# Kernel tuning notes

Hardware: AMD Instinct MI355X
Metric: run time of the kernel (lower is better)

The kernel has to match this reference:

```python
import jax, jax.numpy as jnp
import numpy as np

B, L, D, H = 4, 1024, 1024, 16
DH = D // H
NEG = -1e9


def setup_inputs() -> dict:
    key = jax.random.key(0)
    ks = jax.random.split(key, 8)
    sequence = jax.random.normal(ks[0], (B, L, D), dtype=jnp.float32)
    # additive padding mask: all tokens valid -> zeros
    padding_mask = jnp.zeros((B, 1, 1, L), dtype=jnp.float32)
    # additive causal dependency mask: -1e9 above the diagonal
    causal = jnp.triu(jnp.full((L, L), NEG, dtype=jnp.float32), k=1)
    dependency_mask = causal[None, None, :, :]
    scale = 1.0 / np.sqrt(D)
    Wq = jax.random.normal(ks[1], (D, D), dtype=jnp.float32) * scale
    Wk = jax.random.normal(ks[2], (D, D), dtype=jnp.float32) * scale
    Wv = jax.random.normal(ks[3], (D, D), dtype=jnp.float32) * scale
    bq = jnp.zeros((D,), dtype=jnp.float32)
    bk = jnp.zeros((D,), dtype=jnp.float32)
    bv = jnp.zeros((D,), dtype=jnp.float32)
    return {"sequence": sequence, "padding_mask": padding_mask,
            "dependency_mask": dependency_mask,
            "Wq": Wq, "bq": bq, "Wk": Wk, "bk": bk, "Wv": Wv, "bv": bv}


def reference(sequence, padding_mask, dependency_mask, Wq, bq, Wk, bk, Wv, bv):
    b, l, d = sequence.shape
    h, dh = H, d // H
    # Q/K/V linear projections (torch Linear: x @ W^T + b)
    q = (sequence @ Wq.T + bq).reshape(b, l, h, dh)
    k = (sequence @ Wk.T + bk).reshape(b, l, h, dh)
    v = (sequence @ Wv.T + bv).reshape(b, l, h, dh)
    # scaled dot-product scores: [B, H, L, L]
    scores = jnp.einsum('blhd,bmhd->bhlm', q, k) / jnp.sqrt(jnp.float32(dh))
    scores = scores + padding_mask + dependency_mask
    attn = jax.nn.softmax(scores, axis=-1)
    # dropout is identity in eval mode (training=False)
    out = jnp.einsum('bhlm,bmhd->blhd', attn, v)
    return out.reshape(b, l, d)
```

## Files before the change

### kernel.cpp

```cpp
#include <hip/hip_runtime.h>
#include <hip/hip_bf16.h>


#define LL 1024

typedef __attribute__((ext_vector_type(8))) short short8;
typedef __attribute__((ext_vector_type(4))) float floatx4;

__device__ __forceinline__ float bf2f(unsigned short u) {
    return __uint_as_float(((unsigned int)u) << 16);
}
__device__ __forceinline__ unsigned short f2bf(float f) {
    unsigned int x = __float_as_uint(f);
    unsigned int r = x + 0x7fffu + ((x >> 16) & 1u);
    return (unsigned short)(r >> 16);
}

#if __has_builtin(__builtin_amdgcn_global_load_lds)
#define HAVE_GLL 1
typedef __attribute__((address_space(1))) unsigned int as1_u32;
typedef __attribute__((address_space(3))) unsigned int as3_u32;
__device__ __forceinline__ void gll16(const void* g, void* l) {
    __builtin_amdgcn_global_load_lds((const as1_u32*)g, (as3_u32*)l, 16, 0, 0);
}
#endif

__global__ __launch_bounds__(256) void conv_in(
    const float* __restrict__ seq, const float* __restrict__ wq,
    const float* __restrict__ wk,  const float* __restrict__ wv,
    const float* __restrict__ bq,  const float* __restrict__ bk,
    const float* __restrict__ bv,  const float* __restrict__ pm,
    unsigned short* __restrict__ ws)
{
    unsigned int t = blockIdx.x * 256u + threadIdx.x;
    const float* src; unsigned int idx; unsigned short* dst; float scale = 1.0f;
    if (t < 4194304u)      { src = seq; idx = t;            dst = ws + 12582912u; }
    else if (t < 5242880u) { src = wq;  idx = t - 4194304u; dst = ws + 16777216u; }
    else if (t < 6291456u) { src = wk;  idx = t - 5242880u; dst = ws + 17825792u; }
    else if (t < 7340032u) { src = wv;  idx = t - 6291456u; dst = ws + 18874368u; }
    else if (t < 7341056u) { src = bq;  idx = t - 7340032u; dst = ws + 20971520u; }
    else if (t < 7342080u) { src = bk;  idx = t - 7341056u; dst = ws + 20972544u; }
    else if (t < 7343104u) { src = bv;  idx = t - 7342080u; dst = ws + 20973568u; }
    else { src = pm; idx = t - 7343104u; dst = ws + 20974592u; scale = 1.4426950f; }
    dst[idx] = f2bf(src[idx] * scale);
}

__global__ __launch_bounds__(256) void qkv_proj(
    const unsigned short* __restrict__ X,
    const unsigned short* __restrict__ Wq, const unsigned short* __restrict__ bq,
    const unsigned short* __restrict__ Wk, const unsigned short* __restrict__ bk,
    const unsigned short* __restrict__ Wv, const unsigned short* __restrict__ bv,
    unsigned short* __restrict__ dst_base)
{
    const int z = blockIdx.z;
    const unsigned short* W    = (z == 0) ? Wq : ((z == 1) ? Wk : Wv);
    const unsigned short* bias = (z == 0) ? bq : ((z == 1) ? bk : bv);
    const float osc = (z == 0) ? 0.18033688f : 1.0f;
    unsigned short* dst = dst_base + (size_t)z * (4096u * 1024u);

    __shared__ __align__(16) unsigned short AsF[8192];
    __shared__ __align__(16) unsigned short BsF[8192];

    const int tid  = threadIdx.x;
    const int lane = tid & 63;
    const int wave = tid >> 6;
    const int quad = lane >> 4, r16 = lane & 15;
    const int wr = wave >> 1, wc = wave & 1;
    const int m0 = blockIdx.x * 128;
    const int n0 = blockIdx.y * 128;

    const int st_r3  = lane >> 3;
    const int st_col = ((lane & 7) ^ st_r3) << 3;

    floatx4 acc[4][4];
#pragma unroll
    for (int i = 0; i < 4; ++i)
#pragma unroll
        for (int j = 0; j < 4; ++j)
#pragma unroll
            for (int r = 0; r < 4; ++r) acc[i][j][r] = 0.f;

    for (int k0 = 0; k0 < 1024; k0 += 64) {
        __syncthreads();
#ifdef HAVE_GLL
#pragma unroll
        for (int c2 = 0; c2 < 4; ++c2) {
            int seg = wave * 4 + c2;
            int row = seg * 8 + st_r3;
            gll16(X + (size_t)(m0 + row) * 1024 + k0 + st_col, &AsF[seg * 512]);
            gll16(W + (size_t)(n0 + row) * 1024 + k0 + st_col, &BsF[seg * 512]);
        }
#else
#pragma unroll
        for (int c2 = 0; c2 < 4; ++c2) {
            int seg = wave * 4 + c2;
            int row = seg * 8 + st_r3;
            *(uint4*)&AsF[seg * 512 + lane * 8] = *(const uint4*)(X + (size_t)(m0 + row) * 1024 + k0 + st_col);
            *(uint4*)&BsF[seg * 512 + lane * 8] = *(const uint4*)(W + (size_t)(n0 + row) * 1024 + k0 + st_col);
        }
#endif
        __syncthreads();

#pragma unroll
        for (int kk = 0; kk < 2; ++kk) {
            const int csw = ((kk * 4 + quad) ^ (r16 & 7)) << 3;
            short8 a[4], b[4];
#pragma unroll
            for (int i = 0; i < 4; ++i)
                a[i] = *(const short8*)&AsF[(wr * 64 + i * 16 + r16) * 64 + csw];
#pragma unroll
            for (int j = 0; j < 4; ++j)
                b[j] = *(const short8*)&BsF[(wc * 64 + j * 16 + r16) * 64 + csw];
#pragma unroll
            for (int i = 0; i < 4; ++i)
#pragma unroll
                for (int j = 0; j < 4; ++j)
                    acc[i][j] = __builtin_amdgcn_mfma_f32_16x16x32_bf16(a[i], b[j], acc[i][j], 0, 0, 0);
        }
    }

#pragma unroll
    for (int j = 0; j < 4; ++j) {
        int n = n0 + wc * 64 + j * 16 + r16;
        float bvf = bf2f(bias[n]);
        int h = n >> 6, d = n & 63;
#pragma unroll
        for (int i = 0; i < 4; ++i) {
            int m_base = m0 + wr * 64 + i * 16 + quad * 4;
            int b = m_base >> 10, l0 = m_base & 1023;
            if (z == 2) {
                ushort4 st;
                st.x = f2bf(acc[i][j][0] + bvf); st.y = f2bf(acc[i][j][1] + bvf);
                st.z = f2bf(acc[i][j][2] + bvf); st.w = f2bf(acc[i][j][3] + bvf);
                *(ushort4*)&dst[(((size_t)(b * 16 + h)) * 64 + d) * 1024 + l0] = st;
            } else {
#pragma unroll
                for (int r = 0; r < 4; ++r)
                    dst[(((size_t)(b * 16 + h)) * 1024 + (l0 + r)) * 64 + d] =
                        f2bf((acc[i][j][r] + bvf) * osc);
            }
        }
    }
}

__global__ __launch_bounds__(256) void attn(
    const unsigned short* __restrict__ Qw,
    const unsigned short* __restrict__ Kw,
    const unsigned short* __restrict__ Vt_g,
    const unsigned short* __restrict__ pmask,
    float* __restrict__ out)
{
    __shared__ __align__(16) unsigned short KsF[8192];
    __shared__ __align__(16) unsigned short VsF[8192];
    __shared__ __align__(16) unsigned short PsF[4][2048];

    const int tid  = threadIdx.x;
    const int lane = tid & 63;
    const int wave = tid >> 6;
    const int quad = lane >> 4, r16 = lane & 15;

    const int bid  = blockIdx.x;
    const int half = bid >> 8, rr = bid & 255;
    const int bh   = half * 32 + (rr >> 3);
    const int qi   = half ? (7 - (rr & 7)) : (rr & 7);
    const int b    = bh >> 4, h = bh & 15;
    const int q0   = qi << 7;

    const size_t base = (size_t)bh * (1024 * 64);
    const unsigned short* Qg = Qw + base;
    const unsigned short* Kg = Kw + base;
    const unsigned short* Vg = Vt_g + base;

    const int kst_r3  = lane >> 3;
    const int kst_col = ((lane & 7) ^ kst_r3) << 3;
    const int vst_r   = lane >> 4;

    short8 aq[2][2];
#pragma unroll
    for (int f = 0; f < 2; ++f) {
        int qrow = q0 + f * 64 + wave * 16 + r16;
        aq[f][0] = *(const short8*)(Qg + (size_t)qrow * 64 + quad * 8);
        aq[f][1] = *(const short8*)(Qg + (size_t)qrow * 64 + 32 + quad * 8);
    }

    float lsum[2][4];
    floatx4 o[2][4];
#pragma unroll
    for (int f = 0; f < 2; ++f)
#pragma unroll
        for (int r = 0; r < 4; ++r) lsum[f][r] = 0.f;
#pragma unroll
    for (int f = 0; f < 2; ++f)
#pragma unroll
        for (int j = 0; j < 4; ++j)
#pragma unroll
            for (int r = 0; r < 4; ++r) o[f][j][r] = 0.f;

    for (int kt = 0; kt <= qi; ++kt) {
        __syncthreads();
#ifdef HAVE_GLL
#pragma unroll
        for (int c2 = 0; c2 < 4; ++c2) {
            int seg = wave * 4 + c2;
            int krow = seg * 8 + kst_r3;
            gll16(Kg + (size_t)(kt * 128 + krow) * 64 + kst_col, &KsF[seg * 512]);
            int vrow = seg * 4 + vst_r;
            int vcol = (((lane & 15) ^ (vrow & 7))) << 3;
            gll16(Vg + (size_t)vrow * 1024 + kt * 128 + vcol, &VsF[seg * 512]);
        }
#else
#pragma unroll
        for (int c2 = 0; c2 < 4; ++c2) {
            int seg = wave * 4 + c2;
            int krow = seg * 8 + kst_r3;
            *(uint4*)&KsF[seg * 512 + lane * 8] =
                *(const uint4*)(Kg + (size_t)(kt * 128 + krow) * 64 + kst_col);
            int vrow = seg * 4 + vst_r;
            int vcol = (((lane & 15) ^ (vrow & 7))) << 3;
            *(uint4*)&VsF[seg * 512 + lane * 8] =
                *(const uint4*)(Vg + (size_t)vrow * 1024 + kt * 128 + vcol);
        }
#endif
        __syncthreads();

        float pm2[8];
#pragma unroll
        for (int j = 0; j < 8; ++j)
            pm2[j] = bf2f(pmask[b * LL + kt * 128 + j * 16 + r16]) - 12.0f;

#pragma unroll
        for (int f = 0; f < 2; ++f) {
            floatx4 s[8];
#pragma unroll
            for (int j = 0; j < 8; ++j)
#pragma unroll
                for (int r = 0; r < 4; ++r) s[j][r] = 0.f;
#pragma unroll
            for (int j = 0; j < 8; ++j) {
                short8 bk0 = *(const short8*)&KsF[(j * 16 + r16) * 64 + ((((0 * 4 + quad)) ^ (r16 & 7)) << 3)];
                s[j] = __builtin_amdgcn_mfma_f32_16x16x32_bf16(aq[f][0], bk0, s[j], 0, 0, 0);
                short8 bk1 = *(const short8*)&KsF[(j * 16 + r16) * 64 + ((((1 * 4 + quad)) ^ (r16 & 7)) << 3)];
                s[j] = __builtin_amdgcn_mfma_f32_16x16x32_bf16(aq[f][1], bk1, s[j], 0, 0, 0);
            }

            if (kt == qi) {
                const int my_q = q0 + f * 64 + wave * 16 + quad * 4;
#pragma unroll
                for (int j = 0; j < 8; ++j) {
                    int key = kt * 128 + j * 16 + r16;
#pragma unroll
                    for (int r = 0; r < 4; ++r)
                        if (key > my_q + r) s[j][r] -= 1.0e9f;
                }
            }

            asm volatile("s_waitcnt lgkmcnt(0)" ::: "memory");
#pragma unroll
            for (int j = 0; j < 8; ++j) {
                int key = j * 16 + r16;
                int ab = ((key >> 5) << 9) + (((key >> 3) & 3) << 7) + (key & 7) + (quad << 5);
#pragma unroll
                for (int r = 0; r < 4; ++r) {
                    float p = exp2f(s[j][r] + pm2[j]);
                    lsum[f][r] += p;
                    PsF[wave][ab + (r << 3)] = f2bf(p);
                }
            }
            asm volatile("s_waitcnt lgkmcnt(0)" ::: "memory");

#pragma unroll
            for (int kk4 = 0; kk4 < 4; ++kk4) {
                short8 ap = *(const short8*)&PsF[wave][kk4 * 512 + lane * 8];
#pragma unroll
                for (int j2 = 0; j2 < 4; ++j2) {
                    short8 bv = *(const short8*)&VsF[(j2 * 16 + r16) * 128 + (((kk4 * 4 + quad) ^ (r16 & 7)) << 3)];
                    o[f][j2] = __builtin_amdgcn_mfma_f32_16x16x32_bf16(ap, bv, o[f][j2], 0, 0, 0);
                }
            }
        }
    }

#pragma unroll
    for (int f = 0; f < 2; ++f) {
        float linv[4];
#pragma unroll
        for (int r = 0; r < 4; ++r) {
            float l = lsum[f][r];
            l += __shfl_xor(l, 1);
            l += __shfl_xor(l, 2);
            l += __shfl_xor(l, 4);
            l += __shfl_xor(l, 8);
            linv[r] = 1.0f / fmaxf(l, 1.0e-30f);
        }
        const int my_q = q0 + f * 64 + wave * 16 + quad * 4;
#pragma unroll
        for (int j2 = 0; j2 < 4; ++j2) {
            int d = j2 * 16 + r16;
#pragma unroll
            for (int r = 0; r < 4; ++r) {
                size_t oidx = ((size_t)(b * 1024 + my_q + r)) * 1024 + h * 64 + d;
                out[oidx] = o[f][j2][r] * linv[r];
            }
        }
    }
}

__global__ __launch_bounds__(256) void fill_sentinel_f(float* __restrict__ out,
                                                       float v, unsigned int n)
{
    unsigned int t = blockIdx.x * 256u + threadIdx.x;
    if (t < n) out[t] = v;
}

extern "C" void kernel_launch(void* const* d_in, const int* in_sizes, int n_in,
                              void* d_out, int out_size, void* d_ws, size_t ws_size,
                              hipStream_t stream) {
    bool sizes_ok = (n_in == 9) && in_sizes[0] == 4194304 && in_sizes[1] == 4096 &&
                    in_sizes[2] == 1048576 && in_sizes[3] == 1048576 && in_sizes[4] == 1024 &&
                    in_sizes[5] == 1048576 && in_sizes[6] == 1024 && in_sizes[7] == 1048576 &&
                    in_sizes[8] == 1024 && out_size == 4194304;
    if (!sizes_ok) {
        fill_sentinel_f<<<16384, 256, 0, stream>>>((float*)d_out, 100.0f, 4194304u);
        return;
    }
    if (ws_size < 50331652u) {
        fill_sentinel_f<<<16384, 256, 0, stream>>>((float*)d_out, 200.0f, 4194304u);
        return;
    }

    unsigned short* ws = (unsigned short*)d_ws;

    conv_in<<<28700, 256, 0, stream>>>(
        (const float*)d_in[0], (const float*)d_in[3], (const float*)d_in[5],
        (const float*)d_in[7], (const float*)d_in[4], (const float*)d_in[6],
        (const float*)d_in[8], (const float*)d_in[1], ws);

    const unsigned short* cseq = ws + 12582912u;
    const unsigned short* cwq  = ws + 16777216u;
    const unsigned short* cwk  = ws + 17825792u;
    const unsigned short* cwv  = ws + 18874368u;
    const unsigned short* cbq  = ws + 20971520u;
    const unsigned short* cbk  = ws + 20972544u;
    const unsigned short* cbv  = ws + 20973568u;
    const unsigned short* cpm  = ws + 20974592u;

    dim3 g1(32, 8, 3);
    qkv_proj<<<g1, 256, 0, stream>>>(cseq, cwq, cbq, cwk, cbk, cwv, cbv, ws);

    attn<<<512, 256, 0, stream>>>(ws, ws + 4194304u, ws + 8388608u, cpm, (float*)d_out);
}
```

Baseline: 174.8 us.

## Vectorize input conversion and restructure attention to 64-row tiles without LDS K/V

The fp32-to-bf16 conversion kernel now handles 8 elements per thread with float4 loads and a packed 16-byte store, cutting the launch to about an eighth of the blocks. The attention kernel switches from 128-query blocks with LDS-staged K/V tiles to 64-query blocks on a 2D grid. Each wave loads its K and V MFMA operands directly from global memory into registers, which removes the block-wide barriers. The P tile layout is changed to a padded row-major buffer. The cost is that every wave re-reads K/V from global/L2 instead of sharing them, register pressure rises, and blocks no longer pair causal tiles for load balance.

Result: slower. 264.1 us (+51.1%).

```diff
diff --git a/kernel.cpp b/kernel.cpp
--- a/kernel.cpp
+++ b/kernel.cpp
@@ -33,16 +33,25 @@
     unsigned short* __restrict__ ws)
 {
     unsigned int t = blockIdx.x * 256u + threadIdx.x;
+    if (t >= 918400u) return;
+    unsigned int e = t * 8u;
     const float* src; unsigned int idx; unsigned short* dst; float scale = 1.0f;
-    if (t < 4194304u)      { src = seq; idx = t;            dst = ws + 12582912u; }
-    else if (t < 5242880u) { src = wq;  idx = t - 4194304u; dst = ws + 16777216u; }
-    else if (t < 6291456u) { src = wk;  idx = t - 5242880u; dst = ws + 17825792u; }
-    else if (t < 7340032u) { src = wv;  idx = t - 6291456u; dst = ws + 18874368u; }
-    else if (t < 7341056u) { src = bq;  idx = t - 7340032u; dst = ws + 20971520u; }
-    else if (t < 7342080u) { src = bk;  idx = t - 7341056u; dst = ws + 20972544u; }
-    else if (t < 7343104u) { src = bv;  idx = t - 7342080u; dst = ws + 20973568u; }
-    else { src = pm; idx = t - 7343104u; dst = ws + 20974592u; scale = 1.4426950f; }
-    dst[idx] = f2bf(src[idx] * scale);
+    if (e < 4194304u)      { src = seq; idx = e;            dst = ws + 12582912u; }
+    else if (e < 5242880u) { src = wq;  idx = e - 4194304u; dst = ws + 16777216u; }
+    else if (e < 6291456u) { src = wk;  idx = e - 5242880u; dst = ws + 17825792u; }
+    else if (e < 7340032u) { src = wv;  idx = e - 6291456u; dst = ws + 18874368u; }
+    else if (e < 7341056u) { src = bq;  idx = e - 7340032u; dst = ws + 20971520u; }
+    else if (e < 7342080u) { src = bk;  idx = e - 7341056u; dst = ws + 20972544u; }
+    else if (e < 7343104u) { src = bv;  idx = e - 7342080u; dst = ws + 20973568u; }
+    else { src = pm; idx = e - 7343104u; dst = ws + 20974592u; scale = 1.4426950f; }
+    float4 a = *(const float4*)(src + idx);
+    float4 c = *(const float4*)(src + idx + 4);
+    uint4 st;
+    st.x = (unsigned)f2bf(a.x * scale) | ((unsigned)f2bf(a.y * scale) << 16);
+    st.y = (unsigned)f2bf(a.z * scale) | ((unsigned)f2bf(a.w * scale) << 16);
+    st.z = (unsigned)f2bf(c.x * scale) | ((unsigned)f2bf(c.y * scale) << 16);
+    st.w = (unsigned)f2bf(c.z * scale) | ((unsigned)f2bf(c.w * scale) << 16);
+    *(uint4*)(dst + idx) = st;
 }
 
 __global__ __launch_bounds__(256) void qkv_proj(
@@ -150,157 +159,118 @@
     const unsigned short* __restrict__ pmask,
     float* __restrict__ out)
 {
-    __shared__ __align__(16) unsigned short KsF[8192];
-    __shared__ __align__(16) unsigned short VsF[8192];
-    __shared__ __align__(16) unsigned short PsF[4][2048];
+    __shared__ __align__(16) unsigned short PsF[4][2176];
 
     const int tid  = threadIdx.x;
     const int lane = tid & 63;
     const int wave = tid >> 6;
     const int quad = lane >> 4, r16 = lane & 15;
 
-    const int bid  = blockIdx.x;
-    const int half = bid >> 8, rr = bid & 255;
-    const int bh   = half * 32 + (rr >> 3);
-    const int qi   = half ? (7 - (rr & 7)) : (rr & 7);
-    const int b    = bh >> 4, h = bh & 15;
-    const int q0   = qi << 7;
+    const int qt = blockIdx.x;
+    const int bh = blockIdx.y;
+    const int b  = bh >> 4, h = bh & 15;
+    const int q0 = qt * 64;
 
     const size_t base = (size_t)bh * (1024 * 64);
     const unsigned short* Qg = Qw + base;
     const unsigned short* Kg = Kw + base;
     const unsigned short* Vg = Vt_g + base;
 
-    const int kst_r3  = lane >> 3;
-    const int kst_col = ((lane & 7) ^ kst_r3) << 3;
-    const int vst_r   = lane >> 4;
-
-    short8 aq[2][2];
-#pragma unroll
-    for (int f = 0; f < 2; ++f) {
-        int qrow = q0 + f * 64 + wave * 16 + r16;
-        aq[f][0] = *(const short8*)(Qg + (size_t)qrow * 64 + quad * 8);
-        aq[f][1] = *(const short8*)(Qg + (size_t)qrow * 64 + 32 + quad * 8);
-    }
-
-    float lsum[2][4];
-    floatx4 o[2][4];
-#pragma unroll
-    for (int f = 0; f < 2; ++f)
-#pragma unroll
-        for (int r = 0; r < 4; ++r) lsum[f][r] = 0.f;
-#pragma unroll
-    for (int f = 0; f < 2; ++f)
-#pragma unroll
-        for (int j = 0; j < 4; ++j)
-#pragma unroll
-            for (int r = 0; r < 4; ++r) o[f][j][r] = 0.f;
-
-    for (int kt = 0; kt <= qi; ++kt) {
-        __syncthreads();
-#ifdef HAVE_GLL
-#pragma unroll
-        for (int c2 = 0; c2 < 4; ++c2) {
-            int seg = wave * 4 + c2;
-            int krow = seg * 8 + kst_r3;
-            gll16(Kg + (size_t)(kt * 128 + krow) * 64 + kst_col, &KsF[seg * 512]);
-            int vrow = seg * 4 + vst_r;
-            int vcol = (((lane & 15) ^ (vrow & 7))) << 3;
-            gll16(Vg + (size_t)vrow * 1024 + kt * 128 + vcol, &VsF[seg * 512]);
-        }
-#else
-#pragma unroll
-        for (int c2 = 0; c2 < 4; ++c2) {
-            int seg = wave * 4 + c2;
-            int krow = seg * 8 + kst_r3;
-            *(uint4*)&KsF[seg * 512 + lane * 8] =
-                *(const uint4*)(Kg + (size_t)(kt * 128 + krow) * 64 + kst_col);
-            int vrow = seg * 4 + vst_r;
-            int vcol = (((lane & 15) ^ (vrow & 7))) << 3;
-            *(uint4*)&VsF[seg * 512 + lane * 8] =
-                *(const uint4*)(Vg + (size_t)vrow * 1024 + kt * 128 + vcol);
-        }
-#endif
-        __syncthreads();
+    const int qrow = q0 + wave * 16 + r16;
+    short8 aq0 = *(const short8*)(Qg + (size_t)qrow * 64 + quad * 8);
+    short8 aq1 = *(const short8*)(Qg + (size_t)qrow * 64 + 32 + quad * 8);
+
+    const int my_q = q0 + wave * 16 + quad * 4;
+
+    float lsum[4];
+    floatx4 o[4];
+#pragma unroll
+    for (int r = 0; r < 4; ++r) lsum[r] = 0.f;
+#pragma unroll
+    for (int j2 = 0; j2 < 4; ++j2)
+#pragma unroll
+        for (int r = 0; r < 4; ++r) o[j2][r] = 0.f;
+
+    const int ktmax = qt >> 1;
+    for (int kt = 0; kt <= ktmax; ++kt) {
+        short8 bk[8][2];
+#pragma unroll
+        for (int j = 0; j < 8; ++j)
+#pragma unroll
+            for (int kk = 0; kk < 2; ++kk)
+                bk[j][kk] = *(const short8*)(Kg + (size_t)(kt * 128 + j * 16 + r16) * 64 + kk * 32 + quad * 8);
+
+        floatx4 s[8];
+#pragma unroll
+        for (int j = 0; j < 8; ++j)
+#pragma unroll
+            for (int r = 0; r < 4; ++r) s[j][r] = 0.f;
+#pragma unroll
+        for (int j = 0; j < 8; ++j) {
+            s[j] = __builtin_amdgcn_mfma_f32_16x16x32_bf16(aq0, bk[j][0], s[j], 0, 0, 0);
+            s[j] = __builtin_amdgcn_mfma_f32_16x16x32_bf16(aq1, bk[j][1], s[j], 0, 0, 0);
+        }
+
+        short8 bv[4][4];
+#pragma unroll
+        for (int j2 = 0; j2 < 4; ++j2)
+#pragma unroll
+            for (int kk4 = 0; kk4 < 4; ++kk4)
+                bv[j2][kk4] = *(const short8*)(Vg + (size_t)(j2 * 16 + r16) * 1024 + kt * 128 + kk4 * 32 + quad * 8);
 
         float pm2[8];
 #pragma unroll
         for (int j = 0; j < 8; ++j)
             pm2[j] = bf2f(pmask[b * LL + kt * 128 + j * 16 + r16]) - 12.0f;
 
-#pragma unroll
-        for (int f = 0; f < 2; ++f) {
-            floatx4 s[8];
-#pragma unroll
-            for (int j = 0; j < 8; ++j)
-#pragma unroll
-                for (int r = 0; r < 4; ++r) s[j][r] = 0.f;
+        if (kt == ktmax) {
 #pragma unroll
             for (int j = 0; j < 8; ++j) {
-                short8 bk0 = *(const short8*)&KsF[(j * 16 + r16) * 64 + ((((0 * 4 + quad)) ^ (r16 & 7)) << 3)];
-                s[j] = __builtin_amdgcn_mfma_f32_16x16x32_bf16(aq[f][0], bk0, s[j], 0, 0, 0);
-                short8 bk1 = *(const short8*)&KsF[(j * 16 + r16) * 64 + ((((1 * 4 + quad)) ^ (r16 & 7)) << 3)];
-                s[j] = __builtin_amdgcn_mfma_f32_16x16x32_bf16(aq[f][1], bk1, s[j], 0, 0, 0);
+                int key = kt * 128 + j * 16 + r16;
+#pragma unroll
+                for (int r = 0; r < 4; ++r)
+                    if (key > my_q + r) s[j][r] -= 1.0e9f;
             }
-
-            if (kt == qi) {
-                const int my_q = q0 + f * 64 + wave * 16 + quad * 4;
-#pragma unroll
-                for (int j = 0; j < 8; ++j) {
-                    int key = kt * 128 + j * 16 + r16;
-#pragma unroll
-                    for (int r = 0; r < 4; ++r)
-                        if (key > my_q + r) s[j][r] -= 1.0e9f;
-                }
+        }
+
+        asm volatile("s_waitcnt lgkmcnt(0)" ::: "memory");
+#pragma unroll
+        for (int j = 0; j < 8; ++j) {
+#pragma unroll
+            for (int r = 0; r < 4; ++r) {
+                float p = exp2f(s[j][r] + pm2[j]);
+                lsum[r] += p;
+                PsF[wave][(quad * 4 + r) * 136 + j * 16 + r16] = f2bf(p);
             }
-
-            asm volatile("s_waitcnt lgkmcnt(0)" ::: "memory");
-#pragma unroll
-            for (int j = 0; j < 8; ++j) {
-                int key = j * 16 + r16;
-                int ab = ((key >> 5) << 9) + (((key >> 3) & 3) << 7) + (key & 7) + (quad << 5);
-#pragma unroll
-                for (int r = 0; r < 4; ++r) {
-                    float p = exp2f(s[j][r] + pm2[j]);
-                    lsum[f][r] += p;
-                    PsF[wave][ab + (r << 3)] = f2bf(p);
-                }
-            }
-            asm volatile("s_waitcnt lgkmcnt(0)" ::: "memory");
-
-#pragma unroll
-            for (int kk4 = 0; kk4 < 4; ++kk4) {
-                short8 ap = *(const short8*)&PsF[wave][kk4 * 512 + lane * 8];
-#pragma unroll
-                for (int j2 = 0; j2 < 4; ++j2) {
-                    short8 bv = *(const short8*)&VsF[(j2 * 16 + r16) * 128 + (((kk4 * 4 + quad) ^ (r16 & 7)) << 3)];
-                    o[f][j2] = __builtin_amdgcn_mfma_f32_16x16x32_bf16(ap, bv, o[f][j2], 0, 0, 0);
-                }
-            }
-        }
-    }
-
-#pragma unroll
-    for (int f = 0; f < 2; ++f) {
-        float linv[4];
+        }
+        asm volatile("s_waitcnt lgkmcnt(0)" ::: "memory");
+
+#pragma unroll
+        for (int kk4 = 0; kk4 < 4; ++kk4) {
+            short8 ap = *(const short8*)&PsF[wave][r16 * 136 + kk4 * 32 + quad * 8];
+#pragma unroll
+            for (int j2 = 0; j2 < 4; ++j2)
+                o[j2] = __builtin_amdgcn_mfma_f32_16x16x32_bf16(ap, bv[j2][kk4], o[j2], 0, 0, 0);
+        }
+    }
+
+    float linv[4];
+#pragma unroll
+    for (int r = 0; r < 4; ++r) {
+        float l = lsum[r];
+        l += __shfl_xor(l, 1);
+        l += __shfl_xor(l, 2);
+        l += __shfl_xor(l, 4);
+        l += __shfl_xor(l, 8);
+        linv[r] = 1.0f / fmaxf(l, 1.0e-30f);
+    }
+#pragma unroll
+    for (int j2 = 0; j2 < 4; ++j2) {
+        int d = j2 * 16 + r16;
 #pragma unroll
         for (int r = 0; r < 4; ++r) {
-            float l = lsum[f][r];
-            l += __shfl_xor(l, 1);
-            l += __shfl_xor(l, 2);
-            l += __shfl_xor(l, 4);
-            l += __shfl_xor(l, 8);
-            linv[r] = 1.0f / fmaxf(l, 1.0e-30f);
-        }
-        const int my_q = q0 + f * 64 + wave * 16 + quad * 4;
-#pragma unroll
-        for (int j2 = 0; j2 < 4; ++j2) {
-            int d = j2 * 16 + r16;
-#pragma unroll
-            for (int r = 0; r < 4; ++r) {
-                size_t oidx = ((size_t)(b * 1024 + my_q + r)) * 1024 + h * 64 + d;
-                out[oidx] = o[f][j2][r] * linv[r];
-            }
+            size_t oidx = ((size_t)(b * 1024 + my_q + r)) * 1024 + h * 64 + d;
+            out[oidx] = o[j2][r] * linv[r];
         }
     }
 }
@@ -330,7 +300,7 @@
 
     unsigned short* ws = (unsigned short*)d_ws;
 
-    conv_in<<<28700, 256, 0, stream>>>(
+    conv_in<<<3588, 256, 0, stream>>>(
         (const float*)d_in[0], (const float*)d_in[3], (const float*)d_in[5],
         (const float*)d_in[7], (const float*)d_in[4], (const float*)d_in[6],
         (const float*)d_in[8], (const float*)d_in[1], ws);
@@ -347,5 +317,6 @@
     dim3 g1(32, 8, 3);
     qkv_proj<<<g1, 256, 0, stream>>>(cseq, cwq, cbq, cwk, cbk, cwv, cbv, ws);
 
-    attn<<<512, 256, 0, stream>>>(ws, ws + 4194304u, ws + 8388608u, cpm, (float*)d_out);
-}
+    dim3 g2(16, 64);
+    attn<<<g2, 256, 0, stream>>>(ws, ws + 4194304u, ws + 8388608u, cpm, (float*)d_out);
+}
```
